# Performance work log

Measured on AMD Instinct MI355X. Metric: run time of the kernel, lower is better.

The kernel has to match this reference:

```python
import jax, jax.numpy as jnp
import numpy as np

N_NODES = 50000


def _gcn_conv(h, src, dst, W, b, n_nodes):
    """PyG GCNConv: add self-loops, symmetric deg^{-1/2} normalization,
    linear transform, scatter-add aggregation at target nodes."""
    h = h @ W  # [N, out]
    # self-loops
    loop = jnp.arange(n_nodes, dtype=src.dtype)
    s = jnp.concatenate([src, loop])  # source j
    d = jnp.concatenate([dst, loop])  # target i
    ones = jnp.ones(s.shape[0], dtype=h.dtype)
    deg = jax.ops.segment_sum(ones, d, num_segments=n_nodes)  # in-degree incl. self-loop
    dinv = jnp.where(deg > 0, jax.lax.rsqrt(deg), 0.0)
    norm = dinv[s] * dinv[d]  # [E+N]
    msg = h[s] * norm[:, None]  # gather + scale, [E+N, out]
    out = jax.ops.segment_sum(msg, d, num_segments=n_nodes)  # scatter-add
    return out + b


def reference(x, edge_index, q_emb, W1, b1, W2, b2, Wq, bq):
    src, dst = edge_index[0], edge_index[1]
    n = x.shape[0]
    # dropout rates are 0.0 -> identity
    h1 = jax.nn.relu(_gcn_conv(x, src, dst, W1, b1, n))
    h2 = _gcn_conv(h1, src, dst, W2, b2, n)
    ques = q_emb @ Wq + bq
    return (ques, h2)


def setup_inputs() -> dict:
    key = jax.random.key(0)
    ks = jax.random.split(key, 9)
    d = 128
    sc = 1.0 / np.sqrt(d)
    return {
        "x": jax.random.normal(ks[0], (N_NODES, d), dtype=jnp.float32),
        "edge_index": jax.random.randint(ks[1], (2, 800000), 0, N_NODES, dtype=jnp.int64),
        "q_emb": jax.random.normal(ks[2], (20000, d), dtype=jnp.float32),
        "W1": jax.random.normal(ks[3], (d, d), dtype=jnp.float32) * sc,
        "b1": jax.random.normal(ks[4], (d,), dtype=jnp.float32) * 0.01,
        "W2": jax.random.normal(ks[5], (d, d), dtype=jnp.float32) * sc,
        "b2": jax.random.normal(ks[6], (d,), dtype=jnp.float32) * 0.01,
        "Wq": jax.random.normal(ks[7], (d, d), dtype=jnp.float32) * sc,
        "bq": jax.random.normal(ks[8], (d,), dtype=jnp.float32) * 0.01,
    }
```

## Files before the change

### kernel.cpp

```cpp
#include <hip/hip_runtime.h>

#define D 128
#define NS 8
#define NFB 1024
#define CAP 64

typedef __attribute__((ext_vector_type(8))) short bf16x8;
typedef __attribute__((ext_vector_type(4))) float f32x4;

__device__ __forceinline__ unsigned short f2b(float v) {
    unsigned u = __float_as_uint(v);
    unsigned r = u + 0x7fffu + ((u >> 16) & 1u);
    return (unsigned short)(r >> 16);
}
__device__ __forceinline__ float b2f(unsigned short h) {
    return __uint_as_float(((unsigned)h) << 16);
}


__global__ __launch_bounds__(256) void prep(int* __restrict__ cnt, int N, int nbz,
                                            const float* __restrict__ W1,
                                            const float* __restrict__ W2,
                                            const float* __restrict__ Wq,
                                            unsigned short* __restrict__ o1,
                                            unsigned short* __restrict__ o2,
                                            unsigned short* __restrict__ oq) {
    int b = blockIdx.x;
    if (b < nbz) {
        int idx = b * 256 + threadIdx.x;
        if (idx * 4 + 4 <= N) {
            ((int4*)cnt)[idx] = make_int4(0, 0, 0, 0);
        } else {
            for (int k = idx * 4; k < N; ++k) cnt[k] = 0;
        }
        return;
    }
    int t = (b - nbz) * 256 + threadIdx.x;
    int which = t >> 14;
    int r = t & 16383;
    int n = r >> 7, k = r & 127;
    const float* W = (which == 0) ? W1 : (which == 1) ? W2 : Wq;
    unsigned short* o = (which == 0) ? o1 : (which == 1) ? o2 : oq;
    o[r] = f2b(W[k * D + n]);
}


__device__ __forceinline__ void gemm_body(const float* Af, const unsigned short* Ah,
                                          const unsigned short* Al,
                                          const unsigned short* __restrict__ Wth,
                                          const float* bias, unsigned short* Cb,
                                          float* Cf, int M, int bid, int outf,
                                          char* smem) {
    int lane = threadIdx.x & 63;
    int wave = threadIdx.x >> 6;
    int m16 = (bid * 4 + wave) * 16;
    if (m16 >= M) return;
    int mrow = lane & 15;
    int quad = lane >> 4;

    f32x4 acc[8];
#pragma unroll
    for (int nt = 0; nt < 8; ++nt) acc[nt] = (f32x4){0.f, 0.f, 0.f, 0.f};

    int arow = m16 + mrow;

#pragma unroll
    for (int ks = 0; ks < 4; ++ks) {
        bf16x8 ah, al;
        if (Af) {
            const float* ap = Af + (size_t)arow * D + ks * 32 + quad * 8;
            float4 v0 = *(const float4*)ap;
            float4 v1 = *(const float4*)(ap + 4);
            float vv[8] = {v0.x, v0.y, v0.z, v0.w, v1.x, v1.y, v1.z, v1.w};
#pragma unroll
            for (int j = 0; j < 8; ++j) {
                unsigned short h = f2b(vv[j]);
                ah[j] = (short)h;
                al[j] = (short)f2b(vv[j] - b2f(h));
            }
        } else {
            ah = *(const bf16x8*)(Ah + (size_t)arow * D + ks * 32 + quad * 8);
            al = *(const bf16x8*)(Al + (size_t)arow * D + ks * 32 + quad * 8);
        }
#pragma unroll
        for (int nt = 0; nt < 8; ++nt) {
            bf16x8 wf = *(const bf16x8*)(Wth + (size_t)(nt * 16 + mrow) * D + ks * 32 + quad * 8);
            acc[nt] = __builtin_amdgcn_mfma_f32_16x16x32_bf16(ah, wf, acc[nt], 0, 0, 0);
            acc[nt] = __builtin_amdgcn_mfma_f32_16x16x32_bf16(al, wf, acc[nt], 0, 0, 0);
        }
    }

    if (outf == 0) {
        unsigned short* myl = (unsigned short*)smem + wave * 16 * 136;
#pragma unroll
        for (int nt = 0; nt < 8; ++nt) {
            int col = nt * 16 + mrow;
#pragma unroll
            for (int r = 0; r < 4; ++r)
                myl[(quad * 4 + r) * 136 + col] = f2b(acc[nt][r]);
        }
#pragma unroll
        for (int R = 0; R < 16; ++R) {
            unsigned int v = *(const unsigned int*)&myl[R * 136 + lane * 2];
            ((unsigned int*)(Cb + (size_t)(m16 + R) * D))[lane] = v;
        }
    } else {
#pragma unroll
        for (int nt = 0; nt < 8; ++nt) {
            int col = nt * 16 + mrow;
            float bv = bias[col];
#pragma unroll
            for (int r = 0; r < 4; ++r)
                Cf[(size_t)(m16 + quad * 4 + r) * D + col] = acc[nt][r] + bv;
        }
    }
}

__global__ __launch_bounds__(256) void frontfill(const float* __restrict__ x,
                                                 const float* __restrict__ q,
                                                 const unsigned short* __restrict__ Wth1,
                                                 const unsigned short* __restrict__ Wthq,
                                                 const float* __restrict__ bq,
                                                 unsigned short* __restrict__ Cb,
                                                 float* __restrict__ outq,
                                                 const int* __restrict__ src,
                                                 const int* __restrict__ dst,
                                                 int* __restrict__ cnt,
                                                 int* __restrict__ colv,
                                                 int N, int MQ, int E, int nbN, int nps) {
    __shared__ char smem[4 * 16 * 136 * 2];
    int b = blockIdx.x;
    if (b < NFB) {
        int s = b & (NS - 1);
        int chunk = b >> 3;
        int nchunks = NFB >> 3;
        int lo = s * nps, hi = lo + nps;
        if (hi > N) hi = N;
        int stride = nchunks * 256;
        for (int e = chunk * 256 + threadIdx.x; e < E; e += stride) {
            int d = dst[e];
            if (d >= lo && d < hi) {
                int slot = atomicAdd(&cnt[d], 1);
                if (slot < CAP) colv[(size_t)d * CAP + slot] = src[e];
            }
        }
        return;
    }
    b -= NFB;
    if (b < nbN)
        gemm_body(x, nullptr, nullptr, Wth1, nullptr, Cb, nullptr, N, b, 0, smem);
    else
        gemm_body(q, nullptr, nullptr, Wthq, bq, nullptr, outq, MQ, b - nbN, 1, smem);
}

__global__ __launch_bounds__(256) void gemm2(const unsigned short* __restrict__ Ah,
                                             const unsigned short* __restrict__ Al,
                                             const unsigned short* __restrict__ Wth,
                                             unsigned short* __restrict__ Cb, int M) {
    __shared__ char smem[4 * 16 * 136 * 2];
    gemm_body(nullptr, Ah, Al, Wth, nullptr, Cb, nullptr, M, blockIdx.x, 0, smem);
}

__global__ __launch_bounds__(512) void aggregate(const unsigned short* __restrict__ Tb,
                                                 const int* __restrict__ colv,
                                                 const int* __restrict__ cnt,
                                                 const float* __restrict__ bias,
                                                 float* __restrict__ Of,
                                                 unsigned short* __restrict__ Oh,
                                                 unsigned short* __restrict__ Ol,
                                                 int N, int mode) {
    int wave = threadIdx.x >> 6;
    int lane = threadIdx.x & 63;
    int i = blockIdx.x * 8 + wave;
    if (i >= N) return;
    int g = lane >> 4;
    int l16 = lane & 15;
    const bf16x8* T8 = (const bf16x8*)Tb;

    float acc[8];
#pragma unroll
    for (int k = 0; k < 8; ++k) acc[k] = 0.f;

    int deg = cnt[i];
    int ci = (deg < CAP) ? deg : CAP;
    int e0 = i * CAP;
    int e1 = e0 + ci;
    for (int base = e0; base < e1; base += 64) {
        int cb = e1 - base;
        if (cb > 64) cb = 64;
        int jv = 0;
        float wv = 0.f;
        if (lane < cb) {
            jv = colv[base + lane];
            wv = rsqrtf((float)(cnt[jv] + 1));
        }

        int t = 0;
        for (; t + 16 <= cb; t += 16) {
            int j0 = __shfl(jv, t + g);
            int j1 = __shfl(jv, t + 4 + g);
            int j2 = __shfl(jv, t + 8 + g);
            int j3 = __shfl(jv, t + 12 + g);
            float w0 = __shfl(wv, t + g);
            float w1 = __shfl(wv, t + 4 + g);
            float w2 = __shfl(wv, t + 8 + g);
            float w3 = __shfl(wv, t + 12 + g);
            bf16x8 r0 = T8[(size_t)j0 * 16 + l16];
            bf16x8 r1 = T8[(size_t)j1 * 16 + l16];
            bf16x8 r2 = T8[(size_t)j2 * 16 + l16];
            bf16x8 r3 = T8[(size_t)j3 * 16 + l16];
#pragma unroll
            for (int k = 0; k < 8; ++k) acc[k] = fmaf(w0, b2f((unsigned short)r0[k]), acc[k]);
#pragma unroll
            for (int k = 0; k < 8; ++k) acc[k] = fmaf(w1, b2f((unsigned short)r1[k]), acc[k]);
#pragma unroll
            for (int k = 0; k < 8; ++k) acc[k] = fmaf(w2, b2f((unsigned short)r2[k]), acc[k]);
#pragma unroll
            for (int k = 0; k < 8; ++k) acc[k] = fmaf(w3, b2f((unsigned short)r3[k]), acc[k]);
        }
        for (; t < cb; t += 4) {
            int j = __shfl(jv, t + g);
            float w = __shfl(wv, t + g);
            if (w > 0.f) {
                bf16x8 r = T8[(size_t)j * 16 + l16];
#pragma unroll
                for (int k = 0; k < 8; ++k) acc[k] = fmaf(w, b2f((unsigned short)r[k]), acc[k]);
            }
        }
    }

#pragma unroll
    for (int k = 0; k < 8; ++k) {
        acc[k] += __shfl_xor(acc[k], 16);
        acc[k] += __shfl_xor(acc[k], 32);
    }

    if (g == 0) {
        float di = rsqrtf((float)(deg + 1));
        bf16x8 selfr = T8[(size_t)i * 16 + l16];
        float4 b0 = ((const float4*)bias)[l16 * 2];
        float4 b1v = ((const float4*)bias)[l16 * 2 + 1];
        float bb[8] = {b0.x, b0.y, b0.z, b0.w, b1v.x, b1v.y, b1v.z, b1v.w};
        float res[8];
#pragma unroll
        for (int k = 0; k < 8; ++k)
            res[k] = di * acc[k] + di * di * b2f((unsigned short)selfr[k]) + bb[k];
        if (mode) {
            bf16x8 h, l;
#pragma unroll
            for (int k = 0; k < 8; ++k) {
                float r = fmaxf(res[k], 0.f);
                unsigned short hh = f2b(r);
                h[k] = (short)hh;
                l[k] = (short)f2b(r - b2f(hh));
            }
            ((bf16x8*)Oh)[(size_t)i * 16 + l16] = h;
            ((bf16x8*)Ol)[(size_t)i * 16 + l16] = l;
        } else {
            float4 r0, r1;
            r0.x = res[0]; r0.y = res[1]; r0.z = res[2]; r0.w = res[3];
            r1.x = res[4]; r1.y = res[5]; r1.z = res[6]; r1.w = res[7];
            ((float4*)Of)[(size_t)i * 32 + l16 * 2] = r0;
            ((float4*)Of)[(size_t)i * 32 + l16 * 2 + 1] = r1;
        }
    }
}


static inline char* carve(char*& w, size_t bytes) {
    char* p = w;
    w += (bytes + 255) & ~(size_t)255;
    return p;
}

extern "C" void kernel_launch(void* const* d_in, const int* in_sizes, int n_in,
                              void* d_out, int out_size, void* d_ws, size_t ws_size,
                              hipStream_t stream) {
    const float* x  = (const float*)d_in[0];
    const int*   ei = (const int*)d_in[1];
    const float* q  = (const float*)d_in[2];
    const float* W1 = (const float*)d_in[3];
    const float* b1 = (const float*)d_in[4];
    const float* W2 = (const float*)d_in[5];
    const float* b2 = (const float*)d_in[6];
    const float* Wq = (const float*)d_in[7];
    const float* bq = (const float*)d_in[8];

    int N  = in_sizes[0] / D;
    int E  = in_sizes[1] / 2;
    int MQ = in_sizes[2] / D;

    const int* srcv = ei;
    const int* dstv = ei + E;

    char* w = (char*)d_ws;
    unsigned short* Cb   = (unsigned short*)carve(w, (size_t)N * D * 2);
    unsigned short* Hb   = (unsigned short*)carve(w, (size_t)N * D * 2);
    unsigned short* Lb   = (unsigned short*)carve(w, (size_t)N * D * 2);
    int*            colv = (int*)carve(w, (size_t)N * CAP * 4);
    int*            cnt  = (int*)carve(w, (size_t)N * 4);
    unsigned short* Wth1 = (unsigned short*)carve(w, D * D * 2);
    unsigned short* Wth2 = (unsigned short*)carve(w, D * D * 2);
    unsigned short* Wthq = (unsigned short*)carve(w, D * D * 2);

    float* outq = (float*)d_out;
    float* outh = outq + (size_t)MQ * D;

    int nbz = (N / 4 + 255) / 256;
    int nps = (N + NS - 1) / NS;
    int nbN = (N + 63) / 64;
    int nbQ = (MQ + 63) / 64;

    prep<<<nbz + 192, 256, 0, stream>>>(cnt, N, nbz, W1, W2, Wq, Wth1, Wth2, Wthq);
    frontfill<<<NFB + nbN + nbQ, 256, 0, stream>>>(x, q, Wth1, Wthq, bq, Cb, outq,
                                                   srcv, dstv, cnt, colv,
                                                   N, MQ, E, nbN, nps);

    aggregate<<<(N + 7) / 8, 512, 0, stream>>>(Cb, colv, cnt, b1, nullptr, Hb, Lb, N, 1);

    gemm2<<<nbN, 256, 0, stream>>>(Hb, Lb, Wth2, Cb, N);
    aggregate<<<(N + 7) / 8, 512, 0, stream>>>(Cb, colv, cnt, b2, outh, nullptr, nullptr, N, 0);
}
```

Measured before the change: 258.1 us.

## Fuse layer-1 aggregation with layer-2 GEMM via shared-memory tile

The first aggregation kernel and the separate second GEMM are merged into one kernel. Each 512-thread block aggregates 16 nodes into shared-memory hi/lo bf16 rows, then runs the 16x128 by 128x128 MFMA GEMM and writes the transformed features to a new buffer. This removes the global round trip of the hi/lo intermediates and one kernel launch. In exchange, each wave now aggregates two nodes serially and the block adds syncthreads barriers, which may lower latency hiding in the gather phase.

```diff
diff --git a/kernel.cpp b/kernel.cpp
--- a/kernel.cpp
+++ b/kernel.cpp
@@ -45,8 +45,7 @@
 }
 
 
-__device__ __forceinline__ void gemm_body(const float* Af, const unsigned short* Ah,
-                                          const unsigned short* Al,
+__device__ __forceinline__ void gemm_body(const float* Af,
                                           const unsigned short* __restrict__ Wth,
                                           const float* bias, unsigned short* Cb,
                                           float* Cf, int M, int bid, int outf,
@@ -67,20 +66,15 @@
 #pragma unroll
     for (int ks = 0; ks < 4; ++ks) {
         bf16x8 ah, al;
-        if (Af) {
-            const float* ap = Af + (size_t)arow * D + ks * 32 + quad * 8;
-            float4 v0 = *(const float4*)ap;
-            float4 v1 = *(const float4*)(ap + 4);
-            float vv[8] = {v0.x, v0.y, v0.z, v0.w, v1.x, v1.y, v1.z, v1.w};
-#pragma unroll
-            for (int j = 0; j < 8; ++j) {
-                unsigned short h = f2b(vv[j]);
-                ah[j] = (short)h;
-                al[j] = (short)f2b(vv[j] - b2f(h));
-            }
-        } else {
-            ah = *(const bf16x8*)(Ah + (size_t)arow * D + ks * 32 + quad * 8);
-            al = *(const bf16x8*)(Al + (size_t)arow * D + ks * 32 + quad * 8);
+        const float* ap = Af + (size_t)arow * D + ks * 32 + quad * 8;
+        float4 v0 = *(const float4*)ap;
+        float4 v1 = *(const float4*)(ap + 4);
+        float vv[8] = {v0.x, v0.y, v0.z, v0.w, v1.x, v1.y, v1.z, v1.w};
+#pragma unroll
+        for (int j = 0; j < 8; ++j) {
+            unsigned short h = f2b(vv[j]);
+            ah[j] = (short)h;
+            al[j] = (short)f2b(vv[j] - b2f(h));
         }
 #pragma unroll
         for (int nt = 0; nt < 8; ++nt) {
@@ -148,39 +142,18 @@
     }
     b -= NFB;
     if (b < nbN)
-        gemm_body(x, nullptr, nullptr, Wth1, nullptr, Cb, nullptr, N, b, 0, smem);
+        gemm_body(x, Wth1, nullptr, Cb, nullptr, N, b, 0, smem);
     else
-        gemm_body(q, nullptr, nullptr, Wthq, bq, nullptr, outq, MQ, b - nbN, 1, smem);
-}
-
-__global__ __launch_bounds__(256) void gemm2(const unsigned short* __restrict__ Ah,
-                                             const unsigned short* __restrict__ Al,
-                                             const unsigned short* __restrict__ Wth,
-                                             unsigned short* __restrict__ Cb, int M) {
-    __shared__ char smem[4 * 16 * 136 * 2];
-    gemm_body(nullptr, Ah, Al, Wth, nullptr, Cb, nullptr, M, blockIdx.x, 0, smem);
-}
-
-__global__ __launch_bounds__(512) void aggregate(const unsigned short* __restrict__ Tb,
-                                                 const int* __restrict__ colv,
-                                                 const int* __restrict__ cnt,
-                                                 const float* __restrict__ bias,
-                                                 float* __restrict__ Of,
-                                                 unsigned short* __restrict__ Oh,
-                                                 unsigned short* __restrict__ Ol,
-                                                 int N, int mode) {
-    int wave = threadIdx.x >> 6;
-    int lane = threadIdx.x & 63;
-    int i = blockIdx.x * 8 + wave;
-    if (i >= N) return;
-    int g = lane >> 4;
-    int l16 = lane & 15;
-    const bf16x8* T8 = (const bf16x8*)Tb;
-
-    float acc[8];
+        gemm_body(q, Wthq, bq, nullptr, outq, MQ, b - nbN, 1, smem);
+}
+
+__device__ __forceinline__ void agg_node(const bf16x8* __restrict__ T8,
+                                         const int* __restrict__ colv,
+                                         const int* __restrict__ cnt,
+                                         int i, int lane, int g, int l16,
+                                         float acc[8]) {
 #pragma unroll
     for (int k = 0; k < 8; ++k) acc[k] = 0.f;
-
     int deg = cnt[i];
     int ci = (deg < CAP) ? deg : CAP;
     int e0 = i * CAP;
@@ -194,7 +167,6 @@
             jv = colv[base + lane];
             wv = rsqrtf((float)(cnt[jv] + 1));
         }
-
         int t = 0;
         for (; t + 16 <= cb; t += 16) {
             int j0 = __shfl(jv, t + g);
@@ -228,41 +200,129 @@
             }
         }
     }
-
 #pragma unroll
     for (int k = 0; k < 8; ++k) {
         acc[k] += __shfl_xor(acc[k], 16);
         acc[k] += __shfl_xor(acc[k], 32);
     }
+}
+
+__global__ __launch_bounds__(512) void agg1_gemm(const unsigned short* __restrict__ Tb,
+                                                 const int* __restrict__ colv,
+                                                 const int* __restrict__ cnt,
+                                                 const float* __restrict__ bias,
+                                                 const unsigned short* __restrict__ Wth2,
+                                                 unsigned short* __restrict__ Cb2,
+                                                 int N) {
+    __shared__ unsigned short AH[16 * 136];
+    __shared__ unsigned short AL[16 * 136];
+    int wave = threadIdx.x >> 6;
+    int lane = threadIdx.x & 63;
+    int g = lane >> 4;
+    int l16 = lane & 15;
+    int node0 = blockIdx.x * 16;
+    const bf16x8* T8 = (const bf16x8*)Tb;
+
+#pragma unroll
+    for (int sub = 0; sub < 2; ++sub) {
+        int row = wave * 2 + sub;
+        int i = node0 + row;
+        float acc[8];
+        if (i < N) {
+            agg_node(T8, colv, cnt, i, lane, g, l16, acc);
+            if (g == 0) {
+                int deg = cnt[i];
+                float di = rsqrtf((float)(deg + 1));
+                bf16x8 selfr = T8[(size_t)i * 16 + l16];
+                float4 b0 = ((const float4*)bias)[l16 * 2];
+                float4 b1v = ((const float4*)bias)[l16 * 2 + 1];
+                float bb[8] = {b0.x, b0.y, b0.z, b0.w, b1v.x, b1v.y, b1v.z, b1v.w};
+                bf16x8 h, l;
+#pragma unroll
+                for (int k = 0; k < 8; ++k) {
+                    float r = di * acc[k] + di * di * b2f((unsigned short)selfr[k]) + bb[k];
+                    r = fmaxf(r, 0.f);
+                    unsigned short hh = f2b(r);
+                    h[k] = (short)hh;
+                    l[k] = (short)f2b(r - b2f(hh));
+                }
+                *(bf16x8*)&AH[row * 136 + l16 * 8] = h;
+                *(bf16x8*)&AL[row * 136 + l16 * 8] = l;
+            }
+        } else if (g == 0) {
+            bf16x8 z = (bf16x8){0, 0, 0, 0, 0, 0, 0, 0};
+            *(bf16x8*)&AH[row * 136 + l16 * 8] = z;
+            *(bf16x8*)&AL[row * 136 + l16 * 8] = z;
+        }
+    }
+    __syncthreads();
+
+    int nt = wave;
+    int mrow = l16;
+    int quad = g;
+    f32x4 acc2 = (f32x4){0.f, 0.f, 0.f, 0.f};
+#pragma unroll
+    for (int ks = 0; ks < 4; ++ks) {
+        bf16x8 ah = *(const bf16x8*)&AH[mrow * 136 + ks * 32 + quad * 8];
+        bf16x8 al = *(const bf16x8*)&AL[mrow * 136 + ks * 32 + quad * 8];
+        bf16x8 wf = *(const bf16x8*)(Wth2 + (size_t)(nt * 16 + mrow) * D + ks * 32 + quad * 8);
+        acc2 = __builtin_amdgcn_mfma_f32_16x16x32_bf16(ah, wf, acc2, 0, 0, 0);
+        acc2 = __builtin_amdgcn_mfma_f32_16x16x32_bf16(al, wf, acc2, 0, 0, 0);
+    }
+    __syncthreads();
+    {
+        int col = nt * 16 + mrow;
+#pragma unroll
+        for (int r = 0; r < 4; ++r)
+            AH[(quad * 4 + r) * 136 + col] = f2b(acc2[r]);
+    }
+    __syncthreads();
+#pragma unroll
+    for (int k = 0; k < 2; ++k) {
+        int idx = threadIdx.x + k * 512;
+        int row = idx >> 6;
+        int c = idx & 63;
+        if (node0 + row < N) {
+            unsigned int v = *(const unsigned int*)&AH[row * 136 + c * 2];
+            ((unsigned int*)(Cb2 + (size_t)(node0 + row) * D))[c] = v;
+        }
+    }
+}
+
+__global__ __launch_bounds__(512) void aggregate2(const unsigned short* __restrict__ Tb,
+                                                  const int* __restrict__ colv,
+                                                  const int* __restrict__ cnt,
+                                                  const float* __restrict__ bias,
+                                                  float* __restrict__ Of, int N) {
+    int wave = threadIdx.x >> 6;
+    int lane = threadIdx.x & 63;
+    int i = blockIdx.x * 8 + wave;
+    if (i >= N) return;
+    int g = lane >> 4;
+    int l16 = lane & 15;
+    const bf16x8* T8 = (const bf16x8*)Tb;
+
+    float acc[8];
+    agg_node(T8, colv, cnt, i, lane, g, l16, acc);
 
     if (g == 0) {
+        int deg = cnt[i];
         float di = rsqrtf((float)(deg + 1));
         bf16x8 selfr = T8[(size_t)i * 16 + l16];
         float4 b0 = ((const float4*)bias)[l16 * 2];
         float4 b1v = ((const float4*)bias)[l16 * 2 + 1];
         float bb[8] = {b0.x, b0.y, b0.z, b0.w, b1v.x, b1v.y, b1v.z, b1v.w};
-        float res[8];
-#pragma unroll
-        for (int k = 0; k < 8; ++k)
-            res[k] = di * acc[k] + di * di * b2f((unsigned short)selfr[k]) + bb[k];
-        if (mode) {
-            bf16x8 h, l;
-#pragma unroll
-            for (int k = 0; k < 8; ++k) {
-                float r = fmaxf(res[k], 0.f);
-                unsigned short hh = f2b(r);
-                h[k] = (short)hh;
-                l[k] = (short)f2b(r - b2f(hh));
-            }
-            ((bf16x8*)Oh)[(size_t)i * 16 + l16] = h;
-            ((bf16x8*)Ol)[(size_t)i * 16 + l16] = l;
-        } else {
-            float4 r0, r1;
-            r0.x = res[0]; r0.y = res[1]; r0.z = res[2]; r0.w = res[3];
-            r1.x = res[4]; r1.y = res[5]; r1.z = res[6]; r1.w = res[7];
-            ((float4*)Of)[(size_t)i * 32 + l16 * 2] = r0;
-            ((float4*)Of)[(size_t)i * 32 + l16 * 2 + 1] = r1;
-        }
+        float4 r0, r1;
+        r0.x = di * acc[0] + di * di * b2f((unsigned short)selfr[0]) + bb[0];
+        r0.y = di * acc[1] + di * di * b2f((unsigned short)selfr[1]) + bb[1];
+        r0.z = di * acc[2] + di * di * b2f((unsigned short)selfr[2]) + bb[2];
+        r0.w = di * acc[3] + di * di * b2f((unsigned short)selfr[3]) + bb[3];
+        r1.x = di * acc[4] + di * di * b2f((unsigned short)selfr[4]) + bb[4];
+        r1.y = di * acc[5] + di * di * b2f((unsigned short)selfr[5]) + bb[5];
+        r1.z = di * acc[6] + di * di * b2f((unsigned short)selfr[6]) + bb[6];
+        r1.w = di * acc[7] + di * di * b2f((unsigned short)selfr[7]) + bb[7];
+        ((float4*)Of)[(size_t)i * 32 + l16 * 2] = r0;
+        ((float4*)Of)[(size_t)i * 32 + l16 * 2 + 1] = r1;
     }
 }
 
@@ -295,8 +355,7 @@
 
     char* w = (char*)d_ws;
     unsigned short* Cb   = (unsigned short*)carve(w, (size_t)N * D * 2);
-    unsigned short* Hb   = (unsigned short*)carve(w, (size_t)N * D * 2);
-    unsigned short* Lb   = (unsigned short*)carve(w, (size_t)N * D * 2);
+    unsigned short* Cb2  = (unsigned short*)carve(w, (size_t)N * D * 2);
     int*            colv = (int*)carve(w, (size_t)N * CAP * 4);
     int*            cnt  = (int*)carve(w, (size_t)N * 4);
     unsigned short* Wth1 = (unsigned short*)carve(w, D * D * 2);
@@ -315,9 +374,6 @@
     frontfill<<<NFB + nbN + nbQ, 256, 0, stream>>>(x, q, Wth1, Wthq, bq, Cb, outq,
                                                    srcv, dstv, cnt, colv,
                                                    N, MQ, E, nbN, nps);
-
-    aggregate<<<(N + 7) / 8, 512, 0, stream>>>(Cb, colv, cnt, b1, nullptr, Hb, Lb, N, 1);
-
-    gemm2<<<nbN, 256, 0, stream>>>(Hb, Lb, Wth2, Cb, N);
-    aggregate<<<(N + 7) / 8, 512, 0, stream>>>(Cb, colv, cnt, b2, outh, nullptr, nullptr, N, 0);
-}
+    agg1_gemm<<<(N + 15) / 16, 512, 0, stream>>>(Cb, colv, cnt, b1, Wth2, Cb2, N);
+    aggregate2<<<(N + 7) / 8, 512, 0, stream>>>(Cb2, colv, cnt, b2, outh, N);
+}
```

After: 246.8 us. 1.05x faster.
